# Performance work log

Hardware: AMD Instinct MI355X
Metric: run time of the kernel (lower is better)

## Reference

```python
import jax, jax.numpy as jnp
import numpy as np

NUM_SRC = 200000
NUM_DST = 100000
NUM_EDGES = 1600000
IN_DIM = 128
HID = 256
OUT_DIM = 128


def layer_norm(h, g, b, eps=1e-5):
    mu = jnp.mean(h, axis=-1, keepdims=True)
    var = jnp.mean((h - mu) ** 2, axis=-1, keepdims=True)
    return (h - mu) * jax.lax.rsqrt(var + eps) * g + b


def setup_inputs() -> dict:
    key = jax.random.key(0)
    ks = jax.random.split(key, 8)
    s_in = 1.0 / np.sqrt(IN_DIM)
    s_hid = 1.0 / np.sqrt(HID)
    return {
        "x": jax.random.normal(ks[0], (NUM_SRC, IN_DIM), dtype=jnp.float32),
        "w_l": jax.random.normal(ks[1], (IN_DIM, HID), dtype=jnp.float32) * s_in,
        "b_l": jnp.zeros((HID,), dtype=jnp.float32),
        "w_r": jax.random.normal(ks[2], (IN_DIM, HID), dtype=jnp.float32) * s_in,
        "ln1_g": jnp.ones((HID,), dtype=jnp.float32),
        "ln1_b": jnp.zeros((HID,), dtype=jnp.float32),
        "w_out": jax.random.normal(ks[3], (HID, OUT_DIM), dtype=jnp.float32) * s_hid,
        "b_out": jnp.zeros((OUT_DIM,), dtype=jnp.float32),
        "ln2_g": jnp.ones((OUT_DIM,), dtype=jnp.float32),
        "ln2_b": jnp.zeros((OUT_DIM,), dtype=jnp.float32),
        "edge_src": jax.random.randint(ks[4], (NUM_EDGES,), 0, NUM_SRC, dtype=jnp.int64),
        "edge_dst": jax.random.randint(ks[5], (NUM_EDGES,), 0, NUM_DST, dtype=jnp.int64),
    }


def reference(x, w_l, b_l, w_r, ln1_g, ln1_b, w_out, b_out, ln2_g, ln2_b, edge_src, edge_dst):
    # SAGEConv bipartite: targets are the first NUM_DST rows of x
    x_tgt = x[:NUM_DST]
    # mean aggregation of source-node messages at destination nodes
    msgs = x[edge_src]  # [E, IN_DIM] irregular gather
    summed = jax.ops.segment_sum(msgs, edge_dst, num_segments=NUM_DST)
    cnt = jax.ops.segment_sum(jnp.ones((NUM_EDGES,), dtype=x.dtype), edge_dst, num_segments=NUM_DST)
    mean_nbr = summed / jnp.maximum(cnt, 1.0)[:, None]
    # out = lin_l(aggr) + lin_r(x_target); dropout p=0 is identity
    h = mean_nbr @ w_l + b_l + x_tgt @ w_r
    h = layer_norm(h, ln1_g, ln1_b)
    h = jax.nn.gelu(h, approximate=False)
    out = h @ w_out + b_out
    out = layer_norm(out, ln2_g, ln2_b)
    return out
```

## Files before the change

kernel.cpp:

```cpp
#include <hip/hip_runtime.h>
#include <math.h>

#define NSRC 200000
#define NDST 100000
#define NEDGE 1600000

typedef unsigned int uint32;
typedef unsigned short u16;

typedef short short8 __attribute__((ext_vector_type(8)));
typedef float f32x4 __attribute__((ext_vector_type(4)));

__device__ __forceinline__ u16 f2b(float f) {
  uint32 u = __float_as_uint(f);
  u += 0x7fffu + ((u >> 16) & 1u);
  return (u16)(u >> 16);
}
__device__ __forceinline__ float b2f_lo(uint32 u) { return __uint_as_float(u << 16); }
__device__ __forceinline__ float b2f_hi(uint32 u) { return __uint_as_float(u & 0xffff0000u); }

#define NBKT 1563
#define BKTCAP 1344
#define NB_H 256
#define EPH (NEDGE / NB_H)
#define NB_W 384
#define NB_CVT 25000

__global__ __launch_bounds__(256) void k_prep(const float* __restrict__ x, u16* __restrict__ xb,
                                              const float* __restrict__ wl,
                                              const float* __restrict__ wr,
                                              const float* __restrict__ wo,
                                              u16* __restrict__ wp1f, u16* __restrict__ wp2f,
                                              const int do_cvt, const int* __restrict__ src,
                                              const int* __restrict__ dst,
                                              int* __restrict__ bktcnt,
                                              int* __restrict__ pairs) {
  __shared__ int hist[NBKT];
  __shared__ int loff[NBKT];
  if (blockIdx.x < NB_H) {
    int base = blockIdx.x * EPH;
    for (int i = threadIdx.x; i < NBKT; i += 256) hist[i] = 0;
    __syncthreads();
    for (int i = threadIdx.x; i < EPH; i += 256) atomicAdd(&hist[dst[base + i] >> 6], 1);
    __syncthreads();
    for (int i = threadIdx.x; i < NBKT; i += 256) {
      int h = hist[i];
      loff[i] = h ? atomicAdd(&bktcnt[i * 16], h) : 0;
      hist[i] = 0;
    }
    __syncthreads();
    for (int i = threadIdx.x; i < EPH; i += 256) {
      int d = dst[base + i];
      int s = src[base + i];
      int bin = d >> 6;
      int r = atomicAdd(&hist[bin], 1);
      int pos = loff[bin] + r;
      if (pos < BKTCAP) pairs[(size_t)bin * BKTCAP + pos] = (s << 6) | (d & 63);
    }
    return;
  }
  int bid = blockIdx.x - NB_H;
  if (bid < NB_W) {
    int t = bid * 256 + threadIdx.x;
    if (t < 65536) {
      int j = t & 7, lane = (t >> 3) & 63, nt = (t >> 9) & 3, kc = (t >> 11) & 7, w = t >> 14;
      int k = kc * 32 + (lane >> 4) * 8 + j;
      int n = w * 64 + nt * 16 + (lane & 15);
      float v = (k < 128) ? wl[k * 256 + n] : wr[(k - 128) * 256 + n];
      wp1f[t] = f2b(v);
    } else {
      int t2 = t - 65536;
      int j = t2 & 7, lane = (t2 >> 3) & 63, nt = (t2 >> 9) & 1, kc = (t2 >> 10) & 7, w = t2 >> 13;
      int k = kc * 32 + (lane >> 4) * 8 + j;
      int n = w * 32 + nt * 16 + (lane & 15);
      wp2f[t2] = f2b(wo[k * 128 + n]);
    }
    return;
  }
  if (!do_cvt) return;
  int idx = (bid - NB_W) * 256 + threadIdx.x;
  size_t i = (size_t)idx * 4;
  if (i < (size_t)NSRC * 128) {
    float4 f = *(const float4*)(x + i);
    uint2 o;
    o.x = (uint32)f2b(f.x) | ((uint32)f2b(f.y) << 16);
    o.y = (uint32)f2b(f.z) | ((uint32)f2b(f.w) << 16);
    *(uint2*)(xb + i) = o;
  }
}

#define LDAH 264
#define LCSR_LD 65

__global__ __launch_bounds__(512, 6) void k_fused(
    const u16* __restrict__ xb, const float* __restrict__ xf, const int x_is_bf16,
    const int* __restrict__ pairs, const int* __restrict__ bktcnt,
    const u16* __restrict__ wp1f, const u16* __restrict__ wp2f,
    const float* __restrict__ bl_g, const float* __restrict__ g1_g, const float* __restrict__ b1_g,
    const float* __restrict__ bo_g, const float* __restrict__ g2_g, const float* __restrict__ b2_g,
    float* __restrict__ out) {
  __shared__ __align__(16) u16 AH_lds[64 * LDAH];
  __shared__ float2 stats[8][32];
  __shared__ float2 stats2[64];
  __shared__ int lcnt[64];
  __shared__ int lcsr[64 * LCSR_LD];

  const int tid = threadIdx.x;
  const int wave = tid >> 6;
  const int lane = tid & 63;
  const int l15 = lane & 15;
  const int q = lane >> 4;
  const int wr = wave >> 2;
  const int wc = wave & 3;
  const int row0 = blockIdx.x * 64;

  {
    const int bkt = blockIdx.x;
    int total = bktcnt[(size_t)bkt * 16];
    int mp = total < BKTCAP ? total : BKTCAP;
    if (tid < 64) lcnt[tid] = 0;
    __syncthreads();
    for (int i = tid; i < mp; i += 512) {
      int v = pairs[(size_t)bkt * BKTCAP + i];
      int d6 = v & 63;
      int p = atomicAdd(&lcnt[d6], 1);
      if (p < 64) lcsr[d6 * LCSR_LD + p] = v >> 6;
    }
    __syncthreads();
  }

  {
    const int sub = tid & 15;
    const int dgrp = tid >> 4;
#pragma unroll 1
    for (int pass = 0; pass < 2; pass++) {
      int r = pass * 32 + dgrp;
      int d = row0 + r;
      u16* rowp = AH_lds + r * LDAH;
      if (d < NDST) {
        int n = lcnt[r];
        int m = n < 64 ? n : 64;
        const int* cp = lcsr + r * LCSR_LD;
        float a[8] = {0, 0, 0, 0, 0, 0, 0, 0};
        if (x_is_bf16) {
          int i = 0;
          for (; i + 3 < m; i += 4) {
            uint4 p[4];
#pragma unroll
            for (int u = 0; u < 4; u++)
              p[u] = *(const uint4*)(xb + (size_t)cp[i + u] * 128 + sub * 8);
#pragma unroll
            for (int u = 0; u < 4; u++) {
              a[0] += b2f_lo(p[u].x); a[1] += b2f_hi(p[u].x);
              a[2] += b2f_lo(p[u].y); a[3] += b2f_hi(p[u].y);
              a[4] += b2f_lo(p[u].z); a[5] += b2f_hi(p[u].z);
              a[6] += b2f_lo(p[u].w); a[7] += b2f_hi(p[u].w);
            }
          }
          for (; i < m; i++) {
            uint4 p = *(const uint4*)(xb + (size_t)cp[i] * 128 + sub * 8);
            a[0] += b2f_lo(p.x); a[1] += b2f_hi(p.x);
            a[2] += b2f_lo(p.y); a[3] += b2f_hi(p.y);
            a[4] += b2f_lo(p.z); a[5] += b2f_hi(p.z);
            a[6] += b2f_lo(p.w); a[7] += b2f_hi(p.w);
          }
        } else {
          for (int i = 0; i < m; i++) {
            int s = cp[i];
            const float* p = xf + (size_t)s * 128 + sub * 8;
            float4 f0 = *(const float4*)p;
            float4 f1 = *(const float4*)(p + 4);
            a[0] += f0.x; a[1] += f0.y; a[2] += f0.z; a[3] += f0.w;
            a[4] += f1.x; a[5] += f1.y; a[6] += f1.z; a[7] += f1.w;
          }
        }
        float sc = 1.f / (float)(n > 0 ? n : 1);
        uint4 o;
        o.x = (uint32)f2b(a[0] * sc) | ((uint32)f2b(a[1] * sc) << 16);
        o.y = (uint32)f2b(a[2] * sc) | ((uint32)f2b(a[3] * sc) << 16);
        o.z = (uint32)f2b(a[4] * sc) | ((uint32)f2b(a[5] * sc) << 16);
        o.w = (uint32)f2b(a[6] * sc) | ((uint32)f2b(a[7] * sc) << 16);
        *(uint4*)(rowp + sub * 8) = o;
        uint4 xv;
        if (x_is_bf16) {
          xv = *(const uint4*)(xb + (size_t)d * 128 + sub * 8);
        } else {
          const float* p = xf + (size_t)d * 128 + sub * 8;
          float4 f0 = *(const float4*)p;
          float4 f1 = *(const float4*)(p + 4);
          xv.x = (uint32)f2b(f0.x) | ((uint32)f2b(f0.y) << 16);
          xv.y = (uint32)f2b(f0.z) | ((uint32)f2b(f0.w) << 16);
          xv.z = (uint32)f2b(f1.x) | ((uint32)f2b(f1.y) << 16);
          xv.w = (uint32)f2b(f1.z) | ((uint32)f2b(f1.w) << 16);
        }
        *(uint4*)(rowp + 128 + sub * 8) = xv;
      } else {
        uint4 z = {0u, 0u, 0u, 0u};
        *(uint4*)(rowp + sub * 8) = z;
        *(uint4*)(rowp + 128 + sub * 8) = z;
      }
    }
  }
  __syncthreads();

  f32x4 acc[2][4];
#pragma unroll
  for (int i = 0; i < 2; i++)
#pragma unroll
    for (int j = 0; j < 4; j++) acc[i][j] = (f32x4){0.f, 0.f, 0.f, 0.f};

#pragma unroll 1
  for (int kc = 0; kc < 8; kc++) {
    short8 bfr[4];
    const uint4* bsrc = (const uint4*)(wp1f + (((size_t)wc * 8 + kc) * 4) * 512);
#pragma unroll
    for (int nt = 0; nt < 4; nt++) bfr[nt] = ((const short8*)(bsrc + nt * 64))[lane];
    short8 af[2];
#pragma unroll
    for (int mt = 0; mt < 2; mt++)
      af[mt] = *(const short8*)(AH_lds + (32 * wr + 16 * mt + l15) * LDAH + kc * 32 + q * 8);
#pragma unroll
    for (int mt = 0; mt < 2; mt++)
#pragma unroll
      for (int nt = 0; nt < 4; nt++)
        acc[mt][nt] = __builtin_amdgcn_mfma_f32_16x16x32_bf16(af[mt], bfr[nt], acc[mt][nt], 0, 0, 0);
  }

  float bl[4], g1[4], b1[4];
#pragma unroll
  for (int nt = 0; nt < 4; nt++) {
    int c = 64 * wc + 16 * nt + l15;
    bl[nt] = bl_g[c]; g1[nt] = g1_g[c]; b1[nt] = b1_g[c];
  }
#pragma unroll
  for (int mt = 0; mt < 2; mt++)
#pragma unroll
    for (int nt = 0; nt < 4; nt++)
#pragma unroll
      for (int r = 0; r < 4; r++) acc[mt][nt][r] += bl[nt];

#pragma unroll
  for (int mt = 0; mt < 2; mt++)
#pragma unroll
    for (int r = 0; r < 4; r++) {
      float s = 0.f, s2 = 0.f;
#pragma unroll
      for (int nt = 0; nt < 4; nt++) { float v = acc[mt][nt][r]; s += v; s2 += v * v; }
#pragma unroll
      for (int m = 1; m < 16; m <<= 1) { s += __shfl_xor(s, m, 64); s2 += __shfl_xor(s2, m, 64); }
      if (l15 == 0) stats[wave][16 * mt + 4 * q + r] = make_float2(s, s2);
    }
  __syncthreads();
  if (tid < 64) {
    int wr_ = tid >> 5, rl = tid & 31;
    float S = 0.f, Q = 0.f;
#pragma unroll
    for (int w = 0; w < 4; w++) { float2 t = stats[wr_ * 4 + w][rl]; S += t.x; Q += t.y; }
    float mu = S * (1.f / 256.f);
    float var = Q * (1.f / 256.f) - mu * mu;
    stats2[tid] = make_float2(mu, rsqrtf(var + 1e-5f));
  }
  __syncthreads();
#pragma unroll
  for (int mt = 0; mt < 2; mt++)
#pragma unroll
    for (int r = 0; r < 4; r++) {
      int row = 32 * wr + 16 * mt + 4 * q + r;
      float2 st = stats2[row];
#pragma unroll
      for (int nt = 0; nt < 4; nt++) {
        float v = acc[mt][nt][r];
        float hn = (v - st.x) * st.y * g1[nt] + b1[nt];
        float t2 = hn * hn;
        float u = fmaf(0.044715f * t2, hn, hn);
        float ge = hn / (1.f + __expf(-1.5957691216f * u));
        AH_lds[row * LDAH + 64 * wc + 16 * nt + l15] = f2b(ge);
      }
    }
  __syncthreads();

  f32x4 acc2[2][2];
#pragma unroll
  for (int i = 0; i < 2; i++)
#pragma unroll
    for (int j = 0; j < 2; j++) acc2[i][j] = (f32x4){0.f, 0.f, 0.f, 0.f};

#pragma unroll 1
  for (int kc = 0; kc < 8; kc++) {
    short8 bfr[2];
    const uint4* bsrc = (const uint4*)(wp2f + (((size_t)wc * 8 + kc) * 2) * 512);
#pragma unroll
    for (int nt = 0; nt < 2; nt++) bfr[nt] = ((const short8*)(bsrc + nt * 64))[lane];
    short8 af[2];
#pragma unroll
    for (int mt = 0; mt < 2; mt++)
      af[mt] = *(const short8*)(AH_lds + (32 * wr + 16 * mt + l15) * LDAH + kc * 32 + q * 8);
#pragma unroll
    for (int mt = 0; mt < 2; mt++)
#pragma unroll
      for (int nt = 0; nt < 2; nt++)
        acc2[mt][nt] = __builtin_amdgcn_mfma_f32_16x16x32_bf16(af[mt], bfr[nt], acc2[mt][nt], 0, 0, 0);
  }

  float bo[2], g2[2], b2c[2];
#pragma unroll
  for (int nt = 0; nt < 2; nt++) {
    int c = 32 * wc + 16 * nt + l15;
    bo[nt] = bo_g[c]; g2[nt] = g2_g[c]; b2c[nt] = b2_g[c];
  }
#pragma unroll
  for (int mt = 0; mt < 2; mt++)
#pragma unroll
    for (int nt = 0; nt < 2; nt++)
#pragma unroll
      for (int r = 0; r < 4; r++) acc2[mt][nt][r] += bo[nt];

#pragma unroll
  for (int mt = 0; mt < 2; mt++)
#pragma unroll
    for (int r = 0; r < 4; r++) {
      float s = 0.f, s2 = 0.f;
#pragma unroll
      for (int nt = 0; nt < 2; nt++) { float v = acc2[mt][nt][r]; s += v; s2 += v * v; }
#pragma unroll
      for (int m = 1; m < 16; m <<= 1) { s += __shfl_xor(s, m, 64); s2 += __shfl_xor(s2, m, 64); }
      if (l15 == 0) stats[wave][16 * mt + 4 * q + r] = make_float2(s, s2);
    }
  __syncthreads();
  if (tid < 64) {
    int wr_ = tid >> 5, rl = tid & 31;
    float S = 0.f, Q = 0.f;
#pragma unroll
    for (int w = 0; w < 4; w++) { float2 t = stats[wr_ * 4 + w][rl]; S += t.x; Q += t.y; }
    float mu = S * (1.f / 128.f);
    float var = Q * (1.f / 128.f) - mu * mu;
    stats2[tid] = make_float2(mu, rsqrtf(var + 1e-5f));
  }
  __syncthreads();
#pragma unroll
  for (int mt = 0; mt < 2; mt++)
#pragma unroll
    for (int r = 0; r < 4; r++) {
      int row = 32 * wr + 16 * mt + 4 * q + r;
      int R = row0 + row;
      if (R < NDST) {
        float2 st = stats2[row];
#pragma unroll
        for (int nt = 0; nt < 2; nt++) {
          float v = acc2[mt][nt][r];
          out[(size_t)R * 128 + 32 * wc + 16 * nt + l15] = (v - st.x) * st.y * g2[nt] + b2c[nt];
        }
      }
    }
}

extern "C" void kernel_launch(void* const* d_in, const int* in_sizes, int n_in,
                              void* d_out, int out_size, void* d_ws, size_t ws_size,
                              hipStream_t stream) {
  const float* x   = (const float*)d_in[0];
  const float* w_l = (const float*)d_in[1];
  const float* b_l = (const float*)d_in[2];
  const float* w_r = (const float*)d_in[3];
  const float* g1  = (const float*)d_in[4];
  const float* b1  = (const float*)d_in[5];
  const float* w_o = (const float*)d_in[6];
  const float* b_o = (const float*)d_in[7];
  const float* g2  = (const float*)d_in[8];
  const float* b2  = (const float*)d_in[9];
  const int* esrc  = (const int*)d_in[10];
  const int* edst  = (const int*)d_in[11];
  float* out = (float*)d_out;

  char* ws = (char*)d_ws;
  size_t off = 0;
  auto alloc = [&](size_t bytes) -> void* {
    off = (off + 255) & ~(size_t)255;
    void* p = ws + off;
    off += bytes;
    return p;
  };
  int* bktcnt = (int*)alloc((size_t)NBKT * 16 * 4);
  u16* wp1f   = (u16*)alloc((size_t)65536 * 2);
  u16* wp2f   = (u16*)alloc((size_t)32768 * 2);
  int* pairs  = (int*)alloc((size_t)NBKT * BKTCAP * 4);

  size_t rem = (ws_size > off + 512) ? (ws_size - off - 512) : 0;
  size_t xb_bytes = (size_t)NSRC * 128 * 2;
  int x_is_bf16 = (rem >= xb_bytes) ? 1 : 0;
  u16* xb = x_is_bf16 ? (u16*)alloc(xb_bytes) : nullptr;

  hipMemsetAsync(bktcnt, 0, (size_t)NBKT * 16 * 4, stream);
  k_prep<<<NB_H + NB_W + NB_CVT, 256, 0, stream>>>(x, xb, w_l, w_r, w_o, wp1f, wp2f,
                                                   x_is_bf16, esrc, edst, bktcnt, pairs);
  k_fused<<<NBKT, 512, 0, stream>>>(xb, x, x_is_bf16, pairs, bktcnt, wp1f, wp2f,
                                    b_l, g1, b1, b_o, g2, b2, out);
}
```

Baseline: 337.3 us.

## Halve destination tile to 32 rows per block and rebucket edges by 32

Shrinks the fused kernel tile from 64 to 32 destination rows, so each block runs a single aggregation pass and one MFMA row-tile per wave. Edge bucketing changes to 32-node buckets with a smaller capacity, fewer histogram blocks, and a staggered start for the global bucket atomics. Occupancy hint rises to 8 blocks per CU. The aim is more blocks and less shared memory per block so the gather latency hides better, at the cost of reloading weight fragments for twice as many blocks and dropping the row bounds checks, which relies on NDST dividing evenly by 32.

```diff
diff --git a/kernel.cpp b/kernel.cpp
--- a/kernel.cpp
+++ b/kernel.cpp
@@ -19,9 +19,10 @@
 __device__ __forceinline__ float b2f_lo(uint32 u) { return __uint_as_float(u << 16); }
 __device__ __forceinline__ float b2f_hi(uint32 u) { return __uint_as_float(u & 0xffff0000u); }
 
-#define NBKT 1563
-#define BKTCAP 1344
-#define NB_H 256
+#define TM 32
+#define NBKT 3125
+#define BKTCAP 704
+#define NB_H 64
 #define EPH (NEDGE / NB_H)
 #define NB_W 384
 #define NB_CVT 25000
@@ -41,21 +42,26 @@
     int base = blockIdx.x * EPH;
     for (int i = threadIdx.x; i < NBKT; i += 256) hist[i] = 0;
     __syncthreads();
-    for (int i = threadIdx.x; i < EPH; i += 256) atomicAdd(&hist[dst[base + i] >> 6], 1);
-    __syncthreads();
-    for (int i = threadIdx.x; i < NBKT; i += 256) {
-      int h = hist[i];
-      loff[i] = h ? atomicAdd(&bktcnt[i * 16], h) : 0;
-      hist[i] = 0;
+    for (int i = threadIdx.x; i < EPH; i += 256) atomicAdd(&hist[dst[base + i] >> 5], 1);
+    __syncthreads();
+    {
+      int start = (blockIdx.x * (NBKT / NB_H)) % NBKT;
+      for (int j = threadIdx.x; j < NBKT; j += 256) {
+        int i = j + start;
+        if (i >= NBKT) i -= NBKT;
+        int h = hist[i];
+        loff[i] = h ? atomicAdd(&bktcnt[i * 16], h) : 0;
+        hist[i] = 0;
+      }
     }
     __syncthreads();
     for (int i = threadIdx.x; i < EPH; i += 256) {
       int d = dst[base + i];
       int s = src[base + i];
-      int bin = d >> 6;
+      int bin = d >> 5;
       int r = atomicAdd(&hist[bin], 1);
       int pos = loff[bin] + r;
-      if (pos < BKTCAP) pairs[(size_t)bin * BKTCAP + pos] = (s << 6) | (d & 63);
+      if (pos < BKTCAP) pairs[(size_t)bin * BKTCAP + pos] = (s << 5) | (d & 31);
     }
     return;
   }
@@ -92,18 +98,18 @@
 #define LDAH 264
 #define LCSR_LD 65
 
-__global__ __launch_bounds__(512, 6) void k_fused(
+__global__ __launch_bounds__(512, 8) void k_fused(
     const u16* __restrict__ xb, const float* __restrict__ xf, const int x_is_bf16,
     const int* __restrict__ pairs, const int* __restrict__ bktcnt,
     const u16* __restrict__ wp1f, const u16* __restrict__ wp2f,
     const float* __restrict__ bl_g, const float* __restrict__ g1_g, const float* __restrict__ b1_g,
     const float* __restrict__ bo_g, const float* __restrict__ g2_g, const float* __restrict__ b2_g,
     float* __restrict__ out) {
-  __shared__ __align__(16) u16 AH_lds[64 * LDAH];
-  __shared__ float2 stats[8][32];
-  __shared__ float2 stats2[64];
-  __shared__ int lcnt[64];
-  __shared__ int lcsr[64 * LCSR_LD];
+  __shared__ __align__(16) u16 AH_lds[TM * LDAH];
+  __shared__ float2 stats[8][16];
+  __shared__ float2 stats2[TM];
+  __shared__ int lcnt[TM];
+  __shared__ int lcsr[TM * LCSR_LD];
 
   const int tid = threadIdx.x;
   const int wave = tid >> 6;
@@ -112,102 +118,90 @@
   const int q = lane >> 4;
   const int wr = wave >> 2;
   const int wc = wave & 3;
-  const int row0 = blockIdx.x * 64;
+  const int row0 = blockIdx.x * TM;
 
   {
     const int bkt = blockIdx.x;
     int total = bktcnt[(size_t)bkt * 16];
     int mp = total < BKTCAP ? total : BKTCAP;
-    if (tid < 64) lcnt[tid] = 0;
+    if (tid < TM) lcnt[tid] = 0;
     __syncthreads();
     for (int i = tid; i < mp; i += 512) {
       int v = pairs[(size_t)bkt * BKTCAP + i];
-      int d6 = v & 63;
-      int p = atomicAdd(&lcnt[d6], 1);
-      if (p < 64) lcsr[d6 * LCSR_LD + p] = v >> 6;
+      int d5 = v & 31;
+      int p = atomicAdd(&lcnt[d5], 1);
+      if (p < 64) lcsr[d5 * LCSR_LD + p] = v >> 5;
     }
     __syncthreads();
   }
 
   {
     const int sub = tid & 15;
-    const int dgrp = tid >> 4;
-#pragma unroll 1
-    for (int pass = 0; pass < 2; pass++) {
-      int r = pass * 32 + dgrp;
-      int d = row0 + r;
-      u16* rowp = AH_lds + r * LDAH;
-      if (d < NDST) {
-        int n = lcnt[r];
-        int m = n < 64 ? n : 64;
-        const int* cp = lcsr + r * LCSR_LD;
-        float a[8] = {0, 0, 0, 0, 0, 0, 0, 0};
-        if (x_is_bf16) {
-          int i = 0;
-          for (; i + 3 < m; i += 4) {
-            uint4 p[4];
-#pragma unroll
-            for (int u = 0; u < 4; u++)
-              p[u] = *(const uint4*)(xb + (size_t)cp[i + u] * 128 + sub * 8);
-#pragma unroll
-            for (int u = 0; u < 4; u++) {
-              a[0] += b2f_lo(p[u].x); a[1] += b2f_hi(p[u].x);
-              a[2] += b2f_lo(p[u].y); a[3] += b2f_hi(p[u].y);
-              a[4] += b2f_lo(p[u].z); a[5] += b2f_hi(p[u].z);
-              a[6] += b2f_lo(p[u].w); a[7] += b2f_hi(p[u].w);
-            }
-          }
-          for (; i < m; i++) {
-            uint4 p = *(const uint4*)(xb + (size_t)cp[i] * 128 + sub * 8);
-            a[0] += b2f_lo(p.x); a[1] += b2f_hi(p.x);
-            a[2] += b2f_lo(p.y); a[3] += b2f_hi(p.y);
-            a[4] += b2f_lo(p.z); a[5] += b2f_hi(p.z);
-            a[6] += b2f_lo(p.w); a[7] += b2f_hi(p.w);
-          }
-        } else {
-          for (int i = 0; i < m; i++) {
-            int s = cp[i];
-            const float* p = xf + (size_t)s * 128 + sub * 8;
-            float4 f0 = *(const float4*)p;
-            float4 f1 = *(const float4*)(p + 4);
-            a[0] += f0.x; a[1] += f0.y; a[2] += f0.z; a[3] += f0.w;
-            a[4] += f1.x; a[5] += f1.y; a[6] += f1.z; a[7] += f1.w;
-          }
+    const int r = tid >> 4;
+    const int d = row0 + r;
+    u16* rowp = AH_lds + r * LDAH;
+    int n = lcnt[r];
+    int m = n < 64 ? n : 64;
+    const int* cp = lcsr + r * LCSR_LD;
+    float a[8] = {0, 0, 0, 0, 0, 0, 0, 0};
+    if (x_is_bf16) {
+      int i = 0;
+      for (; i + 3 < m; i += 4) {
+        uint4 p[4];
+#pragma unroll
+        for (int u = 0; u < 4; u++)
+          p[u] = *(const uint4*)(xb + (size_t)cp[i + u] * 128 + sub * 8);
+#pragma unroll
+        for (int u = 0; u < 4; u++) {
+          a[0] += b2f_lo(p[u].x); a[1] += b2f_hi(p[u].x);
+          a[2] += b2f_lo(p[u].y); a[3] += b2f_hi(p[u].y);
+          a[4] += b2f_lo(p[u].z); a[5] += b2f_hi(p[u].z);
+          a[6] += b2f_lo(p[u].w); a[7] += b2f_hi(p[u].w);
         }
-        float sc = 1.f / (float)(n > 0 ? n : 1);
-        uint4 o;
-        o.x = (uint32)f2b(a[0] * sc) | ((uint32)f2b(a[1] * sc) << 16);
-        o.y = (uint32)f2b(a[2] * sc) | ((uint32)f2b(a[3] * sc) << 16);
-        o.z = (uint32)f2b(a[4] * sc) | ((uint32)f2b(a[5] * sc) << 16);
-        o.w = (uint32)f2b(a[6] * sc) | ((uint32)f2b(a[7] * sc) << 16);
-        *(uint4*)(rowp + sub * 8) = o;
-        uint4 xv;
-        if (x_is_bf16) {
-          xv = *(const uint4*)(xb + (size_t)d * 128 + sub * 8);
-        } else {
-          const float* p = xf + (size_t)d * 128 + sub * 8;
-          float4 f0 = *(const float4*)p;
-          float4 f1 = *(const float4*)(p + 4);
-          xv.x = (uint32)f2b(f0.x) | ((uint32)f2b(f0.y) << 16);
-          xv.y = (uint32)f2b(f0.z) | ((uint32)f2b(f0.w) << 16);
-          xv.z = (uint32)f2b(f1.x) | ((uint32)f2b(f1.y) << 16);
-          xv.w = (uint32)f2b(f1.z) | ((uint32)f2b(f1.w) << 16);
-        }
-        *(uint4*)(rowp + 128 + sub * 8) = xv;
-      } else {
-        uint4 z = {0u, 0u, 0u, 0u};
-        *(uint4*)(rowp + sub * 8) = z;
-        *(uint4*)(rowp + 128 + sub * 8) = z;
       }
-    }
-  }
-  __syncthreads();
-
-  f32x4 acc[2][4];
-#pragma unroll
-  for (int i = 0; i < 2; i++)
-#pragma unroll
-    for (int j = 0; j < 4; j++) acc[i][j] = (f32x4){0.f, 0.f, 0.f, 0.f};
+      for (; i < m; i++) {
+        uint4 p = *(const uint4*)(xb + (size_t)cp[i] * 128 + sub * 8);
+        a[0] += b2f_lo(p.x); a[1] += b2f_hi(p.x);
+        a[2] += b2f_lo(p.y); a[3] += b2f_hi(p.y);
+        a[4] += b2f_lo(p.z); a[5] += b2f_hi(p.z);
+        a[6] += b2f_lo(p.w); a[7] += b2f_hi(p.w);
+      }
+    } else {
+      for (int i = 0; i < m; i++) {
+        int s = cp[i];
+        const float* p = xf + (size_t)s * 128 + sub * 8;
+        float4 f0 = *(const float4*)p;
+        float4 f1 = *(const float4*)(p + 4);
+        a[0] += f0.x; a[1] += f0.y; a[2] += f0.z; a[3] += f0.w;
+        a[4] += f1.x; a[5] += f1.y; a[6] += f1.z; a[7] += f1.w;
+      }
+    }
+    float sc = 1.f / (float)(n > 0 ? n : 1);
+    uint4 o;
+    o.x = (uint32)f2b(a[0] * sc) | ((uint32)f2b(a[1] * sc) << 16);
+    o.y = (uint32)f2b(a[2] * sc) | ((uint32)f2b(a[3] * sc) << 16);
+    o.z = (uint32)f2b(a[4] * sc) | ((uint32)f2b(a[5] * sc) << 16);
+    o.w = (uint32)f2b(a[6] * sc) | ((uint32)f2b(a[7] * sc) << 16);
+    *(uint4*)(rowp + sub * 8) = o;
+    uint4 xv;
+    if (x_is_bf16) {
+      xv = *(const uint4*)(xb + (size_t)d * 128 + sub * 8);
+    } else {
+      const float* p = xf + (size_t)d * 128 + sub * 8;
+      float4 f0 = *(const float4*)p;
+      float4 f1 = *(const float4*)(p + 4);
+      xv.x = (uint32)f2b(f0.x) | ((uint32)f2b(f0.y) << 16);
+      xv.y = (uint32)f2b(f0.z) | ((uint32)f2b(f0.w) << 16);
+      xv.z = (uint32)f2b(f1.x) | ((uint32)f2b(f1.y) << 16);
+      xv.w = (uint32)f2b(f1.z) | ((uint32)f2b(f1.w) << 16);
+    }
+    *(uint4*)(rowp + 128 + sub * 8) = xv;
+  }
+  __syncthreads();
+
+  f32x4 acc[4];
+#pragma unroll
+  for (int j = 0; j < 4; j++) acc[j] = (f32x4){0.f, 0.f, 0.f, 0.f};
 
 #pragma unroll 1
   for (int kc = 0; kc < 8; kc++) {
@@ -215,15 +209,10 @@
     const uint4* bsrc = (const uint4*)(wp1f + (((size_t)wc * 8 + kc) * 4) * 512);
 #pragma unroll
     for (int nt = 0; nt < 4; nt++) bfr[nt] = ((const short8*)(bsrc + nt * 64))[lane];
-    short8 af[2];
-#pragma unroll
-    for (int mt = 0; mt < 2; mt++)
-      af[mt] = *(const short8*)(AH_lds + (32 * wr + 16 * mt + l15) * LDAH + kc * 32 + q * 8);
-#pragma unroll
-    for (int mt = 0; mt < 2; mt++)
-#pragma unroll
-      for (int nt = 0; nt < 4; nt++)
-        acc[mt][nt] = __builtin_amdgcn_mfma_f32_16x16x32_bf16(af[mt], bfr[nt], acc[mt][nt], 0, 0, 0);
+    short8 af = *(const short8*)(AH_lds + (16 * wr + l15) * LDAH + kc * 32 + q * 8);
+#pragma unroll
+    for (int nt = 0; nt < 4; nt++)
+      acc[nt] = __builtin_amdgcn_mfma_f32_16x16x32_bf16(af, bfr[nt], acc[nt], 0, 0, 0);
   }
 
   float bl[4], g1[4], b1[4];
@@ -233,26 +222,22 @@
     bl[nt] = bl_g[c]; g1[nt] = g1_g[c]; b1[nt] = b1_g[c];
   }
 #pragma unroll
-  for (int mt = 0; mt < 2; mt++)
-#pragma unroll
-    for (int nt = 0; nt < 4; nt++)
-#pragma unroll
-      for (int r = 0; r < 4; r++) acc[mt][nt][r] += bl[nt];
-
-#pragma unroll
-  for (int mt = 0; mt < 2; mt++)
-#pragma unroll
-    for (int r = 0; r < 4; r++) {
-      float s = 0.f, s2 = 0.f;
-#pragma unroll
-      for (int nt = 0; nt < 4; nt++) { float v = acc[mt][nt][r]; s += v; s2 += v * v; }
-#pragma unroll
-      for (int m = 1; m < 16; m <<= 1) { s += __shfl_xor(s, m, 64); s2 += __shfl_xor(s2, m, 64); }
-      if (l15 == 0) stats[wave][16 * mt + 4 * q + r] = make_float2(s, s2);
-    }
-  __syncthreads();
-  if (tid < 64) {
-    int wr_ = tid >> 5, rl = tid & 31;
+  for (int nt = 0; nt < 4; nt++)
+#pragma unroll
+    for (int r = 0; r < 4; r++) acc[nt][r] += bl[nt];
+
+#pragma unroll
+  for (int r = 0; r < 4; r++) {
+    float s = 0.f, s2 = 0.f;
+#pragma unroll
+    for (int nt = 0; nt < 4; nt++) { float v = acc[nt][r]; s += v; s2 += v * v; }
+#pragma unroll
+    for (int m = 1; m < 16; m <<= 1) { s += __shfl_xor(s, m, 64); s2 += __shfl_xor(s2, m, 64); }
+    if (l15 == 0) stats[wave][4 * q + r] = make_float2(s, s2);
+  }
+  __syncthreads();
+  if (tid < TM) {
+    int wr_ = tid >> 4, rl = tid & 15;
     float S = 0.f, Q = 0.f;
 #pragma unroll
     for (int w = 0; w < 4; w++) { float2 t = stats[wr_ * 4 + w][rl]; S += t.x; Q += t.y; }
@@ -262,28 +247,24 @@
   }
   __syncthreads();
 #pragma unroll
-  for (int mt = 0; mt < 2; mt++)
-#pragma unroll
-    for (int r = 0; r < 4; r++) {
-      int row = 32 * wr + 16 * mt + 4 * q + r;
-      float2 st = stats2[row];
-#pragma unroll
-      for (int nt = 0; nt < 4; nt++) {
-        float v = acc[mt][nt][r];
-        float hn = (v - st.x) * st.y * g1[nt] + b1[nt];
-        float t2 = hn * hn;
-        float u = fmaf(0.044715f * t2, hn, hn);
-        float ge = hn / (1.f + __expf(-1.5957691216f * u));
-        AH_lds[row * LDAH + 64 * wc + 16 * nt + l15] = f2b(ge);
-      }
-    }
-  __syncthreads();
-
-  f32x4 acc2[2][2];
-#pragma unroll
-  for (int i = 0; i < 2; i++)
-#pragma unroll
-    for (int j = 0; j < 2; j++) acc2[i][j] = (f32x4){0.f, 0.f, 0.f, 0.f};
+  for (int r = 0; r < 4; r++) {
+    int row = 16 * wr + 4 * q + r;
+    float2 st = stats2[row];
+#pragma unroll
+    for (int nt = 0; nt < 4; nt++) {
+      float v = acc[nt][r];
+      float hn = (v - st.x) * st.y * g1[nt] + b1[nt];
+      float t2 = hn * hn;
+      float u = fmaf(0.044715f * t2, hn, hn);
+      float ge = hn / (1.f + __expf(-1.5957691216f * u));
+      AH_lds[row * LDAH + 64 * wc + 16 * nt + l15] = f2b(ge);
+    }
+  }
+  __syncthreads();
+
+  f32x4 acc2[2];
+#pragma unroll
+  for (int j = 0; j < 2; j++) acc2[j] = (f32x4){0.f, 0.f, 0.f, 0.f};
 
 #pragma unroll 1
   for (int kc = 0; kc < 8; kc++) {
@@ -291,15 +272,10 @@
     const uint4* bsrc = (const uint4*)(wp2f + (((size_t)wc * 8 + kc) * 2) * 512);
 #pragma unroll
     for (int nt = 0; nt < 2; nt++) bfr[nt] = ((const short8*)(bsrc + nt * 64))[lane];
-    short8 af[2];
-#pragma unroll
-    for (int mt = 0; mt < 2; mt++)
-      af[mt] = *(const short8*)(AH_lds + (32 * wr + 16 * mt + l15) * LDAH + kc * 32 + q * 8);
-#pragma unroll
-    for (int mt = 0; mt < 2; mt++)
-#pragma unroll
-      for (int nt = 0; nt < 2; nt++)
-        acc2[mt][nt] = __builtin_amdgcn_mfma_f32_16x16x32_bf16(af[mt], bfr[nt], acc2[mt][nt], 0, 0, 0);
+    short8 af = *(const short8*)(AH_lds + (16 * wr + l15) * LDAH + kc * 32 + q * 8);
+#pragma unroll
+    for (int nt = 0; nt < 2; nt++)
+      acc2[nt] = __builtin_amdgcn_mfma_f32_16x16x32_bf16(af, bfr[nt], acc2[nt], 0, 0, 0);
   }
 
   float bo[2], g2[2], b2c[2];
@@ -309,26 +285,22 @@
     bo[nt] = bo_g[c]; g2[nt] = g2_g[c]; b2c[nt] = b2_g[c];
   }
 #pragma unroll
-  for (int mt = 0; mt < 2; mt++)
-#pragma unroll
-    for (int nt = 0; nt < 2; nt++)
-#pragma unroll
-      for (int r = 0; r < 4; r++) acc2[mt][nt][r] += bo[nt];
-
-#pragma unroll
-  for (int mt = 0; mt < 2; mt++)
-#pragma unroll
-    for (int r = 0; r < 4; r++) {
-      float s = 0.f, s2 = 0.f;
-#pragma unroll
-      for (int nt = 0; nt < 2; nt++) { float v = acc2[mt][nt][r]; s += v; s2 += v * v; }
-#pragma unroll
-      for (int m = 1; m < 16; m <<= 1) { s += __shfl_xor(s, m, 64); s2 += __shfl_xor(s2, m, 64); }
-      if (l15 == 0) stats[wave][16 * mt + 4 * q + r] = make_float2(s, s2);
-    }
-  __syncthreads();
-  if (tid < 64) {
-    int wr_ = tid >> 5, rl = tid & 31;
+  for (int nt = 0; nt < 2; nt++)
+#pragma unroll
+    for (int r = 0; r < 4; r++) acc2[nt][r] += bo[nt];
+
+#pragma unroll
+  for (int r = 0; r < 4; r++) {
+    float s = 0.f, s2 = 0.f;
+#pragma unroll
+    for (int nt = 0; nt < 2; nt++) { float v = acc2[nt][r]; s += v; s2 += v * v; }
+#pragma unroll
+    for (int m = 1; m < 16; m <<= 1) { s += __shfl_xor(s, m, 64); s2 += __shfl_xor(s2, m, 64); }
+    if (l15 == 0) stats[wave][4 * q + r] = make_float2(s, s2);
+  }
+  __syncthreads();
+  if (tid < TM) {
+    int wr_ = tid >> 4, rl = tid & 15;
     float S = 0.f, Q = 0.f;
 #pragma unroll
     for (int w = 0; w < 4; w++) { float2 t = stats[wr_ * 4 + w][rl]; S += t.x; Q += t.y; }
@@ -338,20 +310,16 @@
   }
   __syncthreads();
 #pragma unroll
-  for (int mt = 0; mt < 2; mt++)
-#pragma unroll
-    for (int r = 0; r < 4; r++) {
-      int row = 32 * wr + 16 * mt + 4 * q + r;
-      int R = row0 + row;
-      if (R < NDST) {
-        float2 st = stats2[row];
-#pragma unroll
-        for (int nt = 0; nt < 2; nt++) {
-          float v = acc2[mt][nt][r];
-          out[(size_t)R * 128 + 32 * wc + 16 * nt + l15] = (v - st.x) * st.y * g2[nt] + b2c[nt];
-        }
-      }
-    }
+  for (int r = 0; r < 4; r++) {
+    int row = 16 * wr + 4 * q + r;
+    float2 st = stats2[row];
+#pragma unroll
+    for (int nt = 0; nt < 2; nt++) {
+      float v = acc2[nt][r];
+      out[(size_t)(row0 + row) * 128 + 32 * wc + 16 * nt + l15] =
+          (v - st.x) * st.y * g2[nt] + b2c[nt];
+    }
+  }
 }
 
 extern "C" void kernel_launch(void* const* d_in, const int* in_sizes, int n_in,
```

New measurement: 409.0 us. 1.21x slower.

## Alias per-row CSR lists into AH_lds, raise occupancy bound, shorten B-fragment lifetimes

Applied to the files above, without the earlier changes.

Drops the separate lcsr shared array and stores each destination row's neighbor index list in that row's slot of AH_lds. The list is read before the aggregated features overwrite the row, which cuts LDS per block so more blocks can be resident. The launch-bounds occupancy hint rises from 6 to 8, and both MFMA loops now load each B fragment right before its two MFMAs instead of holding all of them in registers, to lower VGPR pressure. The tighter register cap risks spills, and correctness relies on the 16 threads of each row group reading the list in lockstep before writing the row.

```diff
diff --git a/kernel.cpp b/kernel.cpp
--- a/kernel.cpp
+++ b/kernel.cpp
@@ -90,9 +90,8 @@
 }
 
 #define LDAH 264
-#define LCSR_LD 65
-
-__global__ __launch_bounds__(512, 6) void k_fused(
+
+__global__ __launch_bounds__(512, 8) void k_fused(
     const u16* __restrict__ xb, const float* __restrict__ xf, const int x_is_bf16,
     const int* __restrict__ pairs, const int* __restrict__ bktcnt,
     const u16* __restrict__ wp1f, const u16* __restrict__ wp2f,
@@ -103,7 +102,6 @@
   __shared__ float2 stats[8][32];
   __shared__ float2 stats2[64];
   __shared__ int lcnt[64];
-  __shared__ int lcsr[64 * LCSR_LD];
 
   const int tid = threadIdx.x;
   const int wave = tid >> 6;
@@ -124,7 +122,7 @@
       int v = pairs[(size_t)bkt * BKTCAP + i];
       int d6 = v & 63;
       int p = atomicAdd(&lcnt[d6], 1);
-      if (p < 64) lcsr[d6 * LCSR_LD + p] = v >> 6;
+      if (p < 64) ((int*)(AH_lds + d6 * LDAH))[p] = v >> 6;
     }
     __syncthreads();
   }
@@ -140,7 +138,7 @@
       if (d < NDST) {
         int n = lcnt[r];
         int m = n < 64 ? n : 64;
-        const int* cp = lcsr + r * LCSR_LD;
+        const int* cp = (const int*)rowp;
         float a[8] = {0, 0, 0, 0, 0, 0, 0, 0};
         if (x_is_bf16) {
           int i = 0;
@@ -211,19 +209,17 @@
 
 #pragma unroll 1
   for (int kc = 0; kc < 8; kc++) {
-    short8 bfr[4];
-    const uint4* bsrc = (const uint4*)(wp1f + (((size_t)wc * 8 + kc) * 4) * 512);
-#pragma unroll
-    for (int nt = 0; nt < 4; nt++) bfr[nt] = ((const short8*)(bsrc + nt * 64))[lane];
     short8 af[2];
 #pragma unroll
     for (int mt = 0; mt < 2; mt++)
       af[mt] = *(const short8*)(AH_lds + (32 * wr + 16 * mt + l15) * LDAH + kc * 32 + q * 8);
-#pragma unroll
-    for (int mt = 0; mt < 2; mt++)
-#pragma unroll
-      for (int nt = 0; nt < 4; nt++)
-        acc[mt][nt] = __builtin_amdgcn_mfma_f32_16x16x32_bf16(af[mt], bfr[nt], acc[mt][nt], 0, 0, 0);
+    const uint4* bsrc = (const uint4*)(wp1f + (((size_t)wc * 8 + kc) * 4) * 512);
+#pragma unroll
+    for (int nt = 0; nt < 4; nt++) {
+      short8 bfr = ((const short8*)(bsrc + nt * 64))[lane];
+      acc[0][nt] = __builtin_amdgcn_mfma_f32_16x16x32_bf16(af[0], bfr, acc[0][nt], 0, 0, 0);
+      acc[1][nt] = __builtin_amdgcn_mfma_f32_16x16x32_bf16(af[1], bfr, acc[1][nt], 0, 0, 0);
+    }
   }
 
   float bl[4], g1[4], b1[4];
@@ -287,19 +283,17 @@
 
 #pragma unroll 1
   for (int kc = 0; kc < 8; kc++) {
-    short8 bfr[2];
-    const uint4* bsrc = (const uint4*)(wp2f + (((size_t)wc * 8 + kc) * 2) * 512);
-#pragma unroll
-    for (int nt = 0; nt < 2; nt++) bfr[nt] = ((const short8*)(bsrc + nt * 64))[lane];
     short8 af[2];
 #pragma unroll
     for (int mt = 0; mt < 2; mt++)
       af[mt] = *(const short8*)(AH_lds + (32 * wr + 16 * mt + l15) * LDAH + kc * 32 + q * 8);
-#pragma unroll
-    for (int mt = 0; mt < 2; mt++)
-#pragma unroll
-      for (int nt = 0; nt < 2; nt++)
-        acc2[mt][nt] = __builtin_amdgcn_mfma_f32_16x16x32_bf16(af[mt], bfr[nt], acc2[mt][nt], 0, 0, 0);
+    const uint4* bsrc = (const uint4*)(wp2f + (((size_t)wc * 8 + kc) * 2) * 512);
+#pragma unroll
+    for (int nt = 0; nt < 2; nt++) {
+      short8 bfr = ((const short8*)(bsrc + nt * 64))[lane];
+      acc2[0][nt] = __builtin_amdgcn_mfma_f32_16x16x32_bf16(af[0], bfr, acc2[0][nt], 0, 0, 0);
+      acc2[1][nt] = __builtin_amdgcn_mfma_f32_16x16x32_bf16(af[1], bfr, acc2[1][nt], 0, 0, 0);
+    }
   }
 
   float bo[2], g2[2], b2c[2];
```

Result: slower. 345.3 us (+2.4%).
